# Kernel tuning notes

Hardware: AMD Instinct MI355X
Metric: run time of the kernel (lower is better)

Reference implementation:

```python
import jax, jax.numpy as jnp
import numpy as np

B, S, H, E, V, P = 64, 1024, 512, 512, 32000, 40


def setup_inputs() -> dict:
    key = jax.random.key(0)
    ks = jax.random.split(key, 18)
    s = 0.05  # weight scale to keep tanh/sigmoid in active range
    inp = {}
    inp["input_token"] = jax.random.randint(ks[0], (B,), 0, V, dtype=jnp.int32)
    inp["hidden"] = jax.random.normal(ks[1], (1, B, H), jnp.float32)
    inp["cell"] = jax.random.normal(ks[2], (1, B, H), jnp.float32)
    inp["encoder_outputs"] = jax.random.normal(ks[3], (B, S, H), jnp.float32)
    pos_ids = jax.random.randint(ks[4], (B, S), 0, P)
    inp["pos_onehot"] = jax.nn.one_hot(pos_ids, P, dtype=jnp.float32)
    inp["src_mask"] = jnp.zeros((B, S), dtype=bool)  # no PAD (avoids all -inf rows)
    # learned parameters (torch Linear convention: y = x @ W.T + b)
    inp["embed_table"] = jax.random.normal(ks[5], (V, E), jnp.float32) * s
    inp["W_s"] = jax.random.normal(ks[6], (H, H), jnp.float32) * s
    inp["W_h"] = jax.random.normal(ks[7], (H, H), jnp.float32) * s
    inp["V_w"] = jax.random.normal(ks[8], (H,), jnp.float32) * s
    inp["W_p"] = jax.random.normal(ks[9], (P,), jnp.float32) * s
    inp["b_p"] = jax.random.normal(ks[10], (), jnp.float32) * s
    inp["W_ih"] = jax.random.normal(ks[11], (4 * H, E + H), jnp.float32) * s
    inp["W_hh"] = jax.random.normal(ks[12], (4 * H, H), jnp.float32) * s
    inp["b_ih"] = jax.random.normal(ks[13], (4 * H,), jnp.float32) * s
    inp["b_hh"] = jax.random.normal(ks[14], (4 * H,), jnp.float32) * s
    inp["W_out"] = jax.random.normal(ks[15], (V, H), jnp.float32) * s
    inp["b_out"] = jax.random.normal(ks[16], (V,), jnp.float32) * s
    return inp


def reference(input_token, hidden, cell, encoder_outputs, pos_onehot, src_mask,
              embed_table, W_s, W_h, V_w, W_p, b_p,
              W_ih, W_hh, b_ih, b_hh, W_out, b_out):
    # embedding (dropout is identity in eval)
    emb = embed_table[input_token]                                  # (B, E)
    q = hidden[-1]                                                  # (B, H)
    # POS-gated Bahdanau attention
    qs = q @ W_s.T                                                  # (B, H)
    eh = jnp.einsum('bsh,kh->bsk', encoder_outputs, W_h)            # (B, S, H)
    energy = jnp.tanh(qs[:, None, :] + eh)                          # (B, S, H)
    scores = jnp.einsum('bsh,h->bs', energy, V_w)                   # (B, S)
    gate = jax.nn.sigmoid(pos_onehot @ W_p + b_p)                   # (B, S)
    gated = jnp.where(src_mask, jnp.float32(-1e30), scores * gate)
    attn = jax.nn.softmax(gated, axis=-1)                           # (B, S)
    context = jnp.einsum('bs,bsh->bh', attn, encoder_outputs)       # (B, H)
    # single-step, single-layer LSTM (torch gate order: i, f, g, o)
    lstm_in = jnp.concatenate([emb, context], axis=-1)              # (B, E+H)
    gates = lstm_in @ W_ih.T + hidden[0] @ W_hh.T + b_ih + b_hh     # (B, 4H)
    i, f, g, o = jnp.split(gates, 4, axis=-1)
    c1 = jax.nn.sigmoid(f) * cell[0] + jax.nn.sigmoid(i) * jnp.tanh(g)
    h1 = jax.nn.sigmoid(o) * jnp.tanh(c1)                           # (B, H)
    pred = h1 @ W_out.T + b_out                                     # (B, V)
    return (pred, h1[None], c1[None], attn)
```

## Files before the change

### kernel.cpp

```cpp
#include <hip/hip_runtime.h>

#define BB 64
#define SS 1024
#define HH 512
#define EE 512
#define VV 32000
#define PP 40

typedef __attribute__((ext_vector_type(8))) __bf16 bf16x8;
typedef __attribute__((ext_vector_type(4))) float f32x4;
typedef __attribute__((ext_vector_type(8))) unsigned short us8_t;
typedef __attribute__((ext_vector_type(4))) unsigned short us4_t;

__device__ inline unsigned short f2bf(float f) {
    unsigned int u = __float_as_uint(f);
    return (unsigned short)((u + 0x7fffu + ((u >> 16) & 1u)) >> 16);
}
__device__ inline float fast_tanh(float x) {
    float e = __expf(-2.0f * fabsf(x));
    float t = (1.0f - e) / (1.0f + e);
    return copysignf(t, x);
}
__device__ inline float sigmf(float x) { return 1.0f / (1.0f + __expf(-x)); }

__device__ inline us8_t pack8(float4 x, float4 y) {
    us8_t u;
    u[0] = f2bf(x.x); u[1] = f2bf(x.y); u[2] = f2bf(x.z); u[3] = f2bf(x.w);
    u[4] = f2bf(y.x); u[5] = f2bf(y.y); u[6] = f2bf(y.z); u[7] = f2bf(y.w);
    return u;
}

__global__ __launch_bounds__(256)
void k_prep(const float* __restrict__ hidden, const float* __restrict__ Ws,
            const float* __restrict__ Wh, const float* __restrict__ pos,
            const float* __restrict__ Wp, const float* __restrict__ bp,
            unsigned short* __restrict__ wh16, float* __restrict__ qs,
            float* __restrict__ gate, float* __restrict__ ctx) {
    int blk = blockIdx.x, t = threadIdx.x;
    if (blk < 64) {
        __shared__ float hb[HH];
        int b = blk;
        for (int i = t; i < HH; i += 256) hb[i] = hidden[b * HH + i];
        __syncthreads();
        for (int n = t; n < HH; n += 256) {
            const float* wr = Ws + (size_t)n * HH;
            float acc = 0.0f;
#pragma unroll 4
            for (int k = 0; k < HH; k += 4) {
                float4 w = *(const float4*)(wr + k);
                acc += w.x * hb[k] + w.y * hb[k + 1] + w.z * hb[k + 2] + w.w * hb[k + 3];
            }
            qs[b * HH + n] = acc;
        }
    } else if (blk < 96) {
        int base = (blk - 64) * 8192 + t * 4;
#pragma unroll
        for (int j = 0; j < 8; ++j) {
            int idx = base + j * 1024;
            float4 x = *(const float4*)(Wh + idx);
            us4_t v;
            v[0] = f2bf(x.x); v[1] = f2bf(x.y); v[2] = f2bf(x.z); v[3] = f2bf(x.w);
            *(us4_t*)(wh16 + idx) = v;
        }
    } else if (blk < 352) {
        int idx = (blk - 96) * 256 + t;
        const float* pr = pos + (size_t)idx * PP;
        float acc = bp[0];
#pragma unroll
        for (int j = 0; j < 10; ++j) {
            float4 x = *(const float4*)(pr + j * 4);
            acc += x.x * Wp[j * 4] + x.y * Wp[j * 4 + 1] + x.z * Wp[j * 4 + 2] + x.w * Wp[j * 4 + 3];
        }
        gate[idx] = sigmf(acc);
    } else {
        int idx = (blk - 352) * 256 + t;
#pragma unroll
        for (int j = 0; j < 16; ++j) ctx[idx * 16 + j] = 0.0f;
    }
}

__global__ __launch_bounds__(512, 2)
void k_scores(const float* __restrict__ enc, const unsigned short* __restrict__ wh16,
              const float* __restrict__ qs, const float* __restrict__ Vw,
              float* __restrict__ part) {
    __shared__ unsigned short tile[2][8192];
    __shared__ float pbuf[8][128];
    int bid = blockIdx.x;
    int nh = bid >> 9, rest = bid & 511;
    int b = rest >> 3, sc = rest & 7;
    int s0 = sc * 128;
    int w = threadIdx.x >> 6, lane = threadIdx.x & 63;
    int l15 = lane & 15, lq = lane >> 4;
    int n0w = nh * 256 + w * 32;

    us8_t areg[2][16];
    const unsigned short* abase = wh16 + (size_t)(n0w + l15) * 512 + lq * 8;
#pragma unroll
    for (int nf = 0; nf < 2; ++nf)
#pragma unroll
        for (int ks = 0; ks < 16; ++ks)
            areg[nf][ks] = *(const us8_t*)(abase + nf * 16 * 512 + ks * 32);

    float qv[2][4], vw[2][4];
#pragma unroll
    for (int nf = 0; nf < 2; ++nf)
#pragma unroll
        for (int r = 0; r < 4; ++r) {
            int n = n0w + nf * 16 + lq * 4 + r;
            qv[nf][r] = qs[b * HH + n];
            vw[nf][r] = Vw[n];
        }

    int sr = threadIdx.x >> 5, seg = threadIdx.x & 31;
    const float* gsrc = enc + ((size_t)(b * SS + s0 + sr)) * HH + seg * 16;
    int slot1 = (seg >> 1) * 4 + (seg & 1) * 2;
    int off1 = slot1 * 128 + ((sr ^ (slot1 & 15)) & 15) * 8;
    int off2 = (slot1 + 1) * 128 + ((sr ^ ((slot1 + 1) & 15)) & 15) * 8;

    float4 x0 = *(const float4*)(gsrc);
    float4 x1 = *(const float4*)(gsrc + 4);
    float4 x2 = *(const float4*)(gsrc + 8);
    float4 x3 = *(const float4*)(gsrc + 12);
    *(us8_t*)(tile[0] + off1) = pack8(x0, x1);
    *(us8_t*)(tile[0] + off2) = pack8(x2, x3);
    {
        const float* g = gsrc + (size_t)16 * HH;
        x0 = *(const float4*)(g);
        x1 = *(const float4*)(g + 4);
        x2 = *(const float4*)(g + 8);
        x3 = *(const float4*)(g + 12);
    }
    __syncthreads();

    for (int st = 0; st < 8; ++st) {
        const unsigned short* tb = tile[st & 1];
        f32x4 acc0 = {0.f, 0.f, 0.f, 0.f};
        f32x4 acc1 = {0.f, 0.f, 0.f, 0.f};
#pragma unroll
        for (int ks = 0; ks < 16; ++ks) {
            int u = ks * 4 + lq;
            us8_t bf = *(const us8_t*)(tb + u * 128 + ((l15 ^ (u & 15)) & 15) * 8);
            acc0 = __builtin_amdgcn_mfma_f32_16x16x32_bf16(
                __builtin_bit_cast(bf16x8, areg[0][ks]),
                __builtin_bit_cast(bf16x8, bf), acc0, 0, 0, 0);
            acc1 = __builtin_amdgcn_mfma_f32_16x16x32_bf16(
                __builtin_bit_cast(bf16x8, areg[1][ks]),
                __builtin_bit_cast(bf16x8, bf), acc1, 0, 0, 0);
        }
        float p = 0.0f;
#pragma unroll
        for (int r = 0; r < 4; ++r) {
            p += fast_tanh(acc0[r] + qv[0][r]) * vw[0][r];
            p += fast_tanh(acc1[r] + qv[1][r]) * vw[1][r];
        }
        p += __shfl_xor(p, 16, 64);
        p += __shfl_xor(p, 32, 64);
        if (lq == 0) pbuf[w][st * 16 + l15] = p;

        if (st < 7) {
            unsigned short* tn = tile[(st + 1) & 1];
            *(us8_t*)(tn + off1) = pack8(x0, x1);
            *(us8_t*)(tn + off2) = pack8(x2, x3);
            if (st < 6) {
                const float* g = gsrc + (size_t)(st + 2) * 16 * HH;
                x0 = *(const float4*)(g);
                x1 = *(const float4*)(g + 4);
                x2 = *(const float4*)(g + 8);
                x3 = *(const float4*)(g + 12);
            }
        }
        __syncthreads();
    }

    if (threadIdx.x < 128) {
        float s = 0.0f;
#pragma unroll
        for (int ww = 0; ww < 8; ++ww) s += pbuf[ww][threadIdx.x];
        part[nh * (BB * SS) + b * SS + s0 + threadIdx.x] = s;
    }
}

__global__ __launch_bounds__(512)
void k_context(const float* __restrict__ enc, const float* __restrict__ part,
               const float* __restrict__ gate, const unsigned char* __restrict__ mask,
               float* __restrict__ attn, float* __restrict__ ctx) {
    int b = blockIdx.x >> 4, chunk = blockIdx.x & 15;
    int s0 = chunk * 64, t = threadIdx.x;
    int w = t >> 6, ln = t & 63;
    float sum = 0.0f;
#pragma unroll
    for (int j = 0; j < 2; ++j) {
        int s = j * 512 + t;
        float raw = part[b * SS + s] + part[BB * SS + b * SS + s];
        float v = mask[b * SS + s] ? -1e30f : raw * gate[b * SS + s];
        sum += __expf(v);
    }
#pragma unroll
    for (int off = 1; off < 64; off <<= 1) sum += __shfl_xor(sum, off, 64);
    __shared__ float sl[8];
    if (ln == 0) sl[w] = sum;
    __syncthreads();
    float inv = 1.0f / (sl[0] + sl[1] + sl[2] + sl[3] + sl[4] + sl[5] + sl[6] + sl[7]);

    __shared__ float aw[64];
    if (t < 64) {
        int s = s0 + t;
        float raw = part[b * SS + s] + part[BB * SS + b * SS + s];
        float v = mask[b * SS + s] ? -1e30f : raw * gate[b * SS + s];
        float a = __expf(v) * inv;
        aw[t] = a;
        attn[b * SS + s] = a;
    }
    __syncthreads();

    const float* ebase = enc + ((size_t)(b * SS + s0)) * HH + t;
    float a0 = 0, a1 = 0, a2 = 0, a3 = 0;
#pragma unroll 4
    for (int s = 0; s < 64; s += 4) {
        a0 += aw[s] * ebase[(size_t)s * HH];
        a1 += aw[s + 1] * ebase[(size_t)(s + 1) * HH];
        a2 += aw[s + 2] * ebase[(size_t)(s + 2) * HH];
        a3 += aw[s + 3] * ebase[(size_t)(s + 3) * HH];
    }
    atomicAdd(&ctx[b * HH + t], a0 + a1 + a2 + a3);
}

__global__ __launch_bounds__(256)
void k_build(const int* __restrict__ tok, const float* __restrict__ embt,
             const float* __restrict__ ctx, const float* __restrict__ hidden,
             unsigned short* __restrict__ li16, unsigned short* __restrict__ h16v) {
    int b = blockIdx.x, t = threadIdx.x;
    const float* er = embt + (size_t)tok[b] * EE;
    for (int i = t; i < HH; i += 256) {
        li16[b * 1024 + i] = f2bf(er[i]);
        li16[b * 1024 + 512 + i] = f2bf(ctx[b * HH + i]);
        h16v[b * HH + i] = f2bf(hidden[b * HH + i]);
    }
}

__global__ __launch_bounds__(256)
void k_gates(const unsigned short* __restrict__ li16, const unsigned short* __restrict__ h16v,
             const float* __restrict__ Wih, const float* __restrict__ Whh,
             float* __restrict__ gpart) {
    int nt = blockIdx.x >> 2, ksl = blockIdx.x & 3;
    int wave = threadIdx.x >> 6, lane = threadIdx.x & 63;
    int l15 = lane & 15, lq = lane >> 4, k0 = lq * 8;
    int n0w = nt * 128 + wave * 32;
    f32x4 acc[4][2];
#pragma unroll
    for (int mf = 0; mf < 4; ++mf)
#pragma unroll
        for (int nf = 0; nf < 2; ++nf) acc[mf][nf] = (f32x4){0.f, 0.f, 0.f, 0.f};

    for (int ks = 0; ks < 12; ++ks) {
        int kg = ksl * 384 + ks * 32;
        us8_t af[4];
        if (kg < 1024) {
#pragma unroll
            for (int mf = 0; mf < 4; ++mf)
                af[mf] = *(const us8_t*)(li16 + (mf * 16 + l15) * 1024 + kg + k0);
        } else {
#pragma unroll
            for (int mf = 0; mf < 4; ++mf)
                af[mf] = *(const us8_t*)(h16v + (mf * 16 + l15) * 512 + (kg - 1024) + k0);
        }
#pragma unroll
        for (int nf = 0; nf < 2; ++nf) {
            int n = n0w + nf * 16 + l15;
            us8_t bu;
            if (kg < 1024) {
                const float* wr = Wih + (size_t)n * 1024 + kg + k0;
                bu = pack8(*(const float4*)wr, *(const float4*)(wr + 4));
            } else {
                const float* wr = Whh + (size_t)n * 512 + (kg - 1024) + k0;
                bu = pack8(*(const float4*)wr, *(const float4*)(wr + 4));
            }
#pragma unroll
            for (int mf = 0; mf < 4; ++mf)
                acc[mf][nf] = __builtin_amdgcn_mfma_f32_16x16x32_bf16(
                    __builtin_bit_cast(bf16x8, af[mf]),
                    __builtin_bit_cast(bf16x8, bu), acc[mf][nf], 0, 0, 0);
        }
    }
#pragma unroll
    for (int mf = 0; mf < 4; ++mf)
#pragma unroll
        for (int nf = 0; nf < 2; ++nf)
#pragma unroll
            for (int r = 0; r < 4; ++r) {
                int row = mf * 16 + lq * 4 + r;
                int n = n0w + nf * 16 + l15;
                gpart[ksl * (BB * 2048) + row * 2048 + n] = acc[mf][nf][r];
            }
}

__global__ __launch_bounds__(512)
void k_lstm(const float* __restrict__ gpart, const float* __restrict__ bih,
            const float* __restrict__ bhh, const float* __restrict__ cell,
            float* __restrict__ oh, float* __restrict__ oc,
            unsigned short* __restrict__ h116) {
    int b = blockIdx.x, t = threadIdx.x;
    float gi = bih[t] + bhh[t];
    float gf = bih[512 + t] + bhh[512 + t];
    float gg = bih[1024 + t] + bhh[1024 + t];
    float go = bih[1536 + t] + bhh[1536 + t];
#pragma unroll
    for (int ksl = 0; ksl < 4; ++ksl) {
        const float* gp = gpart + ksl * (BB * 2048) + b * 2048;
        gi += gp[t];
        gf += gp[512 + t];
        gg += gp[1024 + t];
        go += gp[1536 + t];
    }
    float c0 = cell[b * HH + t];
    float c1 = sigmf(gf) * c0 + sigmf(gi) * fast_tanh(gg);
    float h1 = sigmf(go) * fast_tanh(c1);
    oh[b * HH + t] = h1;
    oc[b * HH + t] = c1;
    h116[b * HH + t] = f2bf(h1);
}

__global__ __launch_bounds__(512)
void k_pred(const unsigned short* __restrict__ h116, const float* __restrict__ Wout,
            const float* __restrict__ bout, float* __restrict__ pred) {
    int wave = threadIdx.x >> 6, lane = threadIdx.x & 63;
    int l15 = lane & 15, lq = lane >> 4, k0 = lq * 8;
    int n = blockIdx.x * 128 + wave * 16 + l15;
    f32x4 acc[4];
#pragma unroll
    for (int mf = 0; mf < 4; ++mf) acc[mf] = (f32x4){0.f, 0.f, 0.f, 0.f};
    const float* wr = Wout + (size_t)n * HH;
#pragma unroll 4
    for (int ks = 0; ks < 16; ++ks) {
        float4 x = *(const float4*)(wr + ks * 32 + k0);
        float4 y = *(const float4*)(wr + ks * 32 + k0 + 4);
        us8_t bu = pack8(x, y);
#pragma unroll
        for (int mf = 0; mf < 4; ++mf) {
            us8_t au = *(const us8_t*)(h116 + (mf * 16 + l15) * 512 + ks * 32 + k0);
            acc[mf] = __builtin_amdgcn_mfma_f32_16x16x32_bf16(
                __builtin_bit_cast(bf16x8, au),
                __builtin_bit_cast(bf16x8, bu), acc[mf], 0, 0, 0);
        }
    }
    float bo = bout[n];
#pragma unroll
    for (int mf = 0; mf < 4; ++mf)
#pragma unroll
        for (int r = 0; r < 4; ++r) {
            int row = mf * 16 + lq * 4 + r;
            pred[(size_t)row * VV + n] = acc[mf][r] + bo;
        }
}

extern "C" void kernel_launch(void* const* d_in, const int* in_sizes, int n_in,
                              void* d_out, int out_size, void* d_ws, size_t ws_size,
                              hipStream_t stream) {
    const int* tok = (const int*)d_in[0];
    const float* hidden = (const float*)d_in[1];
    const float* cell = (const float*)d_in[2];
    const float* enc = (const float*)d_in[3];
    const float* pos = (const float*)d_in[4];
    const unsigned char* mask = (const unsigned char*)d_in[5];
    const float* embt = (const float*)d_in[6];
    const float* Ws = (const float*)d_in[7];
    const float* Wh = (const float*)d_in[8];
    const float* Vw = (const float*)d_in[9];
    const float* Wp = (const float*)d_in[10];
    const float* bp = (const float*)d_in[11];
    const float* Wih = (const float*)d_in[12];
    const float* Whh = (const float*)d_in[13];
    const float* bih = (const float*)d_in[14];
    const float* bhh = (const float*)d_in[15];
    const float* Wout = (const float*)d_in[16];
    const float* bout = (const float*)d_in[17];

    float* out = (float*)d_out;
    float* pred = out;
    float* out_h = out + 2048000;
    float* out_c = out + 2080768;
    float* attn = out + 2113536;

    char* wsb = (char*)d_ws;
    unsigned short* wh16 = (unsigned short*)(wsb);
    float* qs = (float*)(wsb + (512 << 10));
    float* gate = (float*)(wsb + (640 << 10));
    float* part = (float*)(wsb + (896 << 10));
    float* ctx = (float*)(wsb + (1408 << 10));
    unsigned short* li16 = (unsigned short*)(wsb + (1536 << 10));
    unsigned short* h16v = (unsigned short*)(wsb + (1664 << 10));
    float* gpart = (float*)(wsb + (1728 << 10));
    unsigned short* h116 = (unsigned short*)(wsb + (3776 << 10));

    hipLaunchKernelGGL(k_prep, dim3(360), dim3(256), 0, stream,
                       hidden, Ws, Wh, pos, Wp, bp, wh16, qs, gate, ctx);
    hipLaunchKernelGGL(k_scores, dim3(1024), dim3(512), 0, stream,
                       enc, wh16, qs, Vw, part);
    hipLaunchKernelGGL(k_context, dim3(1024), dim3(512), 0, stream,
                       enc, part, gate, mask, attn, ctx);
    hipLaunchKernelGGL(k_build, dim3(64), dim3(256), 0, stream,
                       tok, embt, ctx, hidden, li16, h16v);
    hipLaunchKernelGGL(k_gates, dim3(64), dim3(256), 0, stream, li16, h16v, Wih, Whh, gpart);
    hipLaunchKernelGGL(k_lstm, dim3(64), dim3(512), 0, stream,
                       gpart, bih, bhh, cell, out_h, out_c, h116);
    hipLaunchKernelGGL(k_pred, dim3(250), dim3(512), 0, stream, h116, Wout, bout, pred);
}
```

Before: 185.7 us.

## Cache bf16 encoder copy in scores kernel for context pass; use hardware bf16 pack

```diff
diff --git a/kernel.cpp b/kernel.cpp
--- a/kernel.cpp
+++ b/kernel.cpp
@@ -12,10 +12,6 @@
 typedef __attribute__((ext_vector_type(8))) unsigned short us8_t;
 typedef __attribute__((ext_vector_type(4))) unsigned short us4_t;
 
-__device__ inline unsigned short f2bf(float f) {
-    unsigned int u = __float_as_uint(f);
-    return (unsigned short)((u + 0x7fffu + ((u >> 16) & 1u)) >> 16);
-}
 __device__ inline float fast_tanh(float x) {
     float e = __expf(-2.0f * fabsf(x));
     float t = (1.0f - e) / (1.0f + e);
@@ -23,11 +19,16 @@
 }
 __device__ inline float sigmf(float x) { return 1.0f / (1.0f + __expf(-x)); }
 
-__device__ inline us8_t pack8(float4 x, float4 y) {
-    us8_t u;
-    u[0] = f2bf(x.x); u[1] = f2bf(x.y); u[2] = f2bf(x.z); u[3] = f2bf(x.w);
-    u[4] = f2bf(y.x); u[5] = f2bf(y.y); u[6] = f2bf(y.z); u[7] = f2bf(y.w);
-    return u;
+__device__ inline unsigned int cvtpk(float lo, float hi) {
+    unsigned int r;
+    asm volatile("v_cvt_pk_bf16_f32 %0, %1, %2" : "=v"(r) : "v"(lo), "v"(hi));
+    return r;
+}
+__device__ inline us8_t pack8c(float4 x, float4 y) {
+    union { unsigned int u[4]; us8_t v; } r;
+    r.u[0] = cvtpk(x.x, x.y); r.u[1] = cvtpk(x.z, x.w);
+    r.u[2] = cvtpk(y.x, y.y); r.u[3] = cvtpk(y.z, y.w);
+    return r.v;
 }
 
 __global__ __launch_bounds__(256)
@@ -58,9 +59,9 @@
         for (int j = 0; j < 8; ++j) {
             int idx = base + j * 1024;
             float4 x = *(const float4*)(Wh + idx);
-            us4_t v;
-            v[0] = f2bf(x.x); v[1] = f2bf(x.y); v[2] = f2bf(x.z); v[3] = f2bf(x.w);
-            *(us4_t*)(wh16 + idx) = v;
+            union { unsigned int u[2]; us4_t v; } r;
+            r.u[0] = cvtpk(x.x, x.y); r.u[1] = cvtpk(x.z, x.w);
+            *(us4_t*)(wh16 + idx) = r.v;
         }
     } else if (blk < 352) {
         int idx = (blk - 96) * 256 + t;
@@ -79,10 +80,11 @@
     }
 }
 
-__global__ __launch_bounds__(512, 2)
+__global__ __launch_bounds__(512)
+__attribute__((amdgpu_waves_per_eu(2, 2)))
 void k_scores(const float* __restrict__ enc, const unsigned short* __restrict__ wh16,
               const float* __restrict__ qs, const float* __restrict__ Vw,
-              float* __restrict__ part) {
+              float* __restrict__ part, unsigned short* __restrict__ enc16, int do16) {
     __shared__ unsigned short tile[2][8192];
     __shared__ float pbuf[8][128];
     int bid = blockIdx.x;
@@ -116,13 +118,19 @@
     int slot1 = (seg >> 1) * 4 + (seg & 1) * 2;
     int off1 = slot1 * 128 + ((sr ^ (slot1 & 15)) & 15) * 8;
     int off2 = (slot1 + 1) * 128 + ((sr ^ ((slot1 + 1) & 15)) & 15) * 8;
+    bool dow = (do16 != 0) && (nh == 0);
+    unsigned short* e16base = enc16 + ((size_t)(b * SS + s0 + sr)) * HH + seg * 16;
 
     float4 x0 = *(const float4*)(gsrc);
     float4 x1 = *(const float4*)(gsrc + 4);
     float4 x2 = *(const float4*)(gsrc + 8);
     float4 x3 = *(const float4*)(gsrc + 12);
-    *(us8_t*)(tile[0] + off1) = pack8(x0, x1);
-    *(us8_t*)(tile[0] + off2) = pack8(x2, x3);
+    {
+        us8_t va = pack8c(x0, x1), vb = pack8c(x2, x3);
+        *(us8_t*)(tile[0] + off1) = va;
+        *(us8_t*)(tile[0] + off2) = vb;
+        if (dow) { *(us8_t*)(e16base) = va; *(us8_t*)(e16base + 8) = vb; }
+    }
     {
         const float* g = gsrc + (size_t)16 * HH;
         x0 = *(const float4*)(g);
@@ -130,9 +138,19 @@
         x2 = *(const float4*)(g + 8);
         x3 = *(const float4*)(g + 12);
     }
-    __syncthreads();
-
+    asm volatile("s_waitcnt lgkmcnt(0)" ::: "memory");
+    __builtin_amdgcn_s_barrier();
+
+#pragma unroll
     for (int st = 0; st < 8; ++st) {
+        float4 y0, y1, y2, y3;
+        if (st < 6) {
+            const float* g = gsrc + (size_t)(st + 2) * 16 * HH;
+            y0 = *(const float4*)(g);
+            y1 = *(const float4*)(g + 4);
+            y2 = *(const float4*)(g + 8);
+            y3 = *(const float4*)(g + 12);
+        }
         const unsigned short* tb = tile[st & 1];
         f32x4 acc0 = {0.f, 0.f, 0.f, 0.f};
         f32x4 acc1 = {0.f, 0.f, 0.f, 0.f};
@@ -158,18 +176,19 @@
         if (lq == 0) pbuf[w][st * 16 + l15] = p;
 
         if (st < 7) {
-            unsigned short* tn = tile[(st + 1) & 1];
-            *(us8_t*)(tn + off1) = pack8(x0, x1);
-            *(us8_t*)(tn + off2) = pack8(x2, x3);
-            if (st < 6) {
-                const float* g = gsrc + (size_t)(st + 2) * 16 * HH;
-                x0 = *(const float4*)(g);
-                x1 = *(const float4*)(g + 4);
-                x2 = *(const float4*)(g + 8);
-                x3 = *(const float4*)(g + 12);
+            us8_t va = pack8c(x0, x1), vb = pack8c(x2, x3);
+            unsigned short* tn = (unsigned short*)tile[(st + 1) & 1];
+            *(us8_t*)(tn + off1) = va;
+            *(us8_t*)(tn + off2) = vb;
+            if (dow) {
+                unsigned short* e = e16base + (size_t)(st + 1) * 16 * HH;
+                *(us8_t*)(e) = va;
+                *(us8_t*)(e + 8) = vb;
             }
         }
-        __syncthreads();
+        asm volatile("s_waitcnt lgkmcnt(0)" ::: "memory");
+        __builtin_amdgcn_s_barrier();
+        if (st < 6) { x0 = y0; x1 = y1; x2 = y2; x3 = y3; }
     }
 
     if (threadIdx.x < 128) {
@@ -180,27 +199,28 @@
     }
 }
 
-__global__ __launch_bounds__(512)
-void k_context(const float* __restrict__ enc, const float* __restrict__ part,
-               const float* __restrict__ gate, const unsigned char* __restrict__ mask,
+__global__ __launch_bounds__(256)
+void k_context(const float* __restrict__ enc, const unsigned short* __restrict__ enc16,
+               int use16, const float* __restrict__ part, const float* __restrict__ gate,
+               const unsigned char* __restrict__ mask,
                float* __restrict__ attn, float* __restrict__ ctx) {
     int b = blockIdx.x >> 4, chunk = blockIdx.x & 15;
     int s0 = chunk * 64, t = threadIdx.x;
     int w = t >> 6, ln = t & 63;
     float sum = 0.0f;
 #pragma unroll
-    for (int j = 0; j < 2; ++j) {
-        int s = j * 512 + t;
+    for (int j = 0; j < 4; ++j) {
+        int s = j * 256 + t;
         float raw = part[b * SS + s] + part[BB * SS + b * SS + s];
         float v = mask[b * SS + s] ? -1e30f : raw * gate[b * SS + s];
         sum += __expf(v);
     }
 #pragma unroll
     for (int off = 1; off < 64; off <<= 1) sum += __shfl_xor(sum, off, 64);
-    __shared__ float sl[8];
+    __shared__ float sl[4];
     if (ln == 0) sl[w] = sum;
     __syncthreads();
-    float inv = 1.0f / (sl[0] + sl[1] + sl[2] + sl[3] + sl[4] + sl[5] + sl[6] + sl[7]);
+    float inv = 1.0f / (sl[0] + sl[1] + sl[2] + sl[3]);
 
     __shared__ float aw[64];
     if (t < 64) {
@@ -213,16 +233,26 @@
     }
     __syncthreads();
 
-    const float* ebase = enc + ((size_t)(b * SS + s0)) * HH + t;
-    float a0 = 0, a1 = 0, a2 = 0, a3 = 0;
+    float a0 = 0.f, a1 = 0.f;
+    if (use16) {
+        const unsigned short* eb = enc16 + ((size_t)(b * SS + s0)) * HH + 2 * t;
 #pragma unroll 4
-    for (int s = 0; s < 64; s += 4) {
-        a0 += aw[s] * ebase[(size_t)s * HH];
-        a1 += aw[s + 1] * ebase[(size_t)(s + 1) * HH];
-        a2 += aw[s + 2] * ebase[(size_t)(s + 2) * HH];
-        a3 += aw[s + 3] * ebase[(size_t)(s + 3) * HH];
-    }
-    atomicAdd(&ctx[b * HH + t], a0 + a1 + a2 + a3);
+        for (int s = 0; s < 64; ++s) {
+            unsigned int u = *(const unsigned int*)(eb + (size_t)s * HH);
+            a0 += aw[s] * __uint_as_float(u << 16);
+            a1 += aw[s] * __uint_as_float(u & 0xffff0000u);
+        }
+    } else {
+        const float* eb = enc + ((size_t)(b * SS + s0)) * HH + 2 * t;
+#pragma unroll 4
+        for (int s = 0; s < 64; ++s) {
+            float2 u = *(const float2*)(eb + (size_t)s * HH);
+            a0 += aw[s] * u.x;
+            a1 += aw[s] * u.y;
+        }
+    }
+    atomicAdd(&ctx[b * HH + 2 * t], a0);
+    atomicAdd(&ctx[b * HH + 2 * t + 1], a1);
 }
 
 __global__ __launch_bounds__(256)
@@ -231,10 +261,10 @@
              unsigned short* __restrict__ li16, unsigned short* __restrict__ h16v) {
     int b = blockIdx.x, t = threadIdx.x;
     const float* er = embt + (size_t)tok[b] * EE;
-    for (int i = t; i < HH; i += 256) {
-        li16[b * 1024 + i] = f2bf(er[i]);
-        li16[b * 1024 + 512 + i] = f2bf(ctx[b * HH + i]);
-        h16v[b * HH + i] = f2bf(hidden[b * HH + i]);
+    for (int i = 2 * t; i < HH; i += 512) {
+        *(unsigned int*)(li16 + b * 1024 + i) = cvtpk(er[i], er[i + 1]);
+        *(unsigned int*)(li16 + b * 1024 + 512 + i) = cvtpk(ctx[b * HH + i], ctx[b * HH + i + 1]);
+        *(unsigned int*)(h16v + b * HH + i) = cvtpk(hidden[b * HH + i], hidden[b * HH + i + 1]);
     }
 }
 
@@ -270,10 +300,10 @@
             us8_t bu;
             if (kg < 1024) {
                 const float* wr = Wih + (size_t)n * 1024 + kg + k0;
-                bu = pack8(*(const float4*)wr, *(const float4*)(wr + 4));
+                bu = pack8c(*(const float4*)wr, *(const float4*)(wr + 4));
             } else {
                 const float* wr = Whh + (size_t)n * 512 + (kg - 1024) + k0;
-                bu = pack8(*(const float4*)wr, *(const float4*)(wr + 4));
+                bu = pack8c(*(const float4*)wr, *(const float4*)(wr + 4));
             }
 #pragma unroll
             for (int mf = 0; mf < 4; ++mf)
@@ -317,7 +347,7 @@
     float h1 = sigmf(go) * fast_tanh(c1);
     oh[b * HH + t] = h1;
     oc[b * HH + t] = c1;
-    h116[b * HH + t] = f2bf(h1);
+    h116[b * HH + t] = (unsigned short)(cvtpk(h1, h1) & 0xffffu);
 }
 
 __global__ __launch_bounds__(512)
@@ -334,7 +364,7 @@
     for (int ks = 0; ks < 16; ++ks) {
         float4 x = *(const float4*)(wr + ks * 32 + k0);
         float4 y = *(const float4*)(wr + ks * 32 + k0 + 4);
-        us8_t bu = pack8(x, y);
+        us8_t bu = pack8c(x, y);
 #pragma unroll
         for (int mf = 0; mf < 4; ++mf) {
             us8_t au = *(const us8_t*)(h116 + (mf * 16 + l15) * 512 + ks * 32 + k0);
@@ -391,13 +421,18 @@
     unsigned short* h16v = (unsigned short*)(wsb + (1664 << 10));
     float* gpart = (float*)(wsb + (1728 << 10));
     unsigned short* h116 = (unsigned short*)(wsb + (3776 << 10));
+    size_t e16off = (size_t)(3840) << 10;
+    size_t e16need = e16off + (size_t)BB * SS * HH * 2;
+    int use16 = (ws_size >= e16need) ? 1 : 0;
+    unsigned short* enc16 = use16 ? (unsigned short*)(wsb + e16off)
+                                  : (unsigned short*)wsb;
 
     hipLaunchKernelGGL(k_prep, dim3(360), dim3(256), 0, stream,
                        hidden, Ws, Wh, pos, Wp, bp, wh16, qs, gate, ctx);
     hipLaunchKernelGGL(k_scores, dim3(1024), dim3(512), 0, stream,
-                       enc, wh16, qs, Vw, part);
-    hipLaunchKernelGGL(k_context, dim3(1024), dim3(512), 0, stream,
-                       enc, part, gate, mask, attn, ctx);
+                       enc, wh16, qs, Vw, part, enc16, use16);
+    hipLaunchKernelGGL(k_context, dim3(1024), dim3(256), 0, stream,
+                       enc, enc16, use16, part, gate, mask, attn, ctx);
     hipLaunchKernelGGL(k_build, dim3(64), dim3(256), 0, stream,
                        tok, embt, ctx, hidden, li16, h16v);
     hipLaunchKernelGGL(k_gates, dim3(64), dim3(256), 0, stream, li16, h16v, Wih, Whh, gpart);
```

Result: slower. 194.1 us (+4.5%).
